# Kernel optimization log

Hardware: AMD Instinct MI355X
Metric: run time of the kernel (lower is better)

Reference implementation:

```python
import jax, jax.numpy as jnp
import numpy as np
import math

B, C1, H, W, D, NH = 32, 128, 32, 32, 256, 8
KS = 9
GLOBAL_RATIO = 0.0005
K_CH = 8


def setup_inputs() -> dict:
    key = jax.random.key(0)
    ks = jax.random.split(key, 6)
    s = 1.0 / math.sqrt(D)
    return {
        "x": jax.random.normal(ks[0], (B, 1, H, W), jnp.float32),
        "conv_w": jax.random.normal(ks[1], (C1, 1, KS, KS), jnp.float32) * 0.05,
        "channel_embed": jax.random.normal(ks[2], (C1, D), jnp.float32),
        "in_proj_w": jax.random.normal(ks[3], (3 * D, D), jnp.float32) * s,
        "in_proj_b": jnp.zeros((3 * D,), jnp.float32),
        "out_proj_w": jax.random.normal(ks[4], (D, D), jnp.float32) * s,
        "out_proj_b": jnp.zeros((D,), jnp.float32),
    }


def _pos_encoding(h, w, d):
    # Faithful to the torch code: the (H, d/2) sin/cos source broadcasts against
    # the trailing (W, d/2) dims of the (H,W,d/2) slice, so the PE varies only
    # along the W axis (requires H == W, which holds here).
    div = jnp.exp(jnp.arange(0, d, 2, dtype=jnp.float32) * (-math.log(10000.0) / d))
    ang = jnp.arange(w, dtype=jnp.float32)[:, None] * div          # (W, d/2)
    pe_w = jnp.stack([jnp.sin(ang), jnp.cos(ang)], axis=-1).reshape(w, d)
    return jnp.broadcast_to(pe_w[None], (h, w, d))                 # (H, W, d)


def _forward(x, conv_w, channel_embed, in_proj_w, in_proj_b, out_proj_w, out_proj_b):
    A = jax.nn.relu(jax.lax.conv_general_dilated(
        x, conv_w, window_strides=(1, 1),
        padding=[(KS // 2, KS // 2), (KS // 2, KS // 2)],
        dimension_numbers=("NCHW", "OIHW", "NCHW")))                # (B,C,H,W)
    Bb, C, Hh, Ww = A.shape
    k = max(1, int(math.ceil(GLOBAL_RATIO * C * Hh * Ww)))          # = 66

    # global top-k threshold mask over flattened activations
    A_flat = A.reshape(Bb, -1)
    topk_vals, _ = jax.lax.top_k(A_flat, k)
    thresh = topk_vals[:, -1][:, None]
    mask_global = (A_flat >= thresh).reshape(A.shape)
    A_global = A * mask_global.astype(A.dtype)

    # per-pixel channel top-8 + scatter
    v = jnp.transpose(A_global, (0, 2, 3, 1))                       # (B,H,W,C)
    topv, topi = jax.lax.top_k(v, K_CH)                             # (B,H,W,8)
    logits = (jax.nn.one_hot(topi, C, dtype=v.dtype) * topv[..., None]).sum(axis=-2)

    # global max normalization per batch element
    gmax = jnp.max(logits.reshape(Bb, -1), axis=1)[:, None, None, None]
    denom = jnp.where(gmax == 0, jnp.float32(1.0), gmax)
    sparse_weights = jnp.where(gmax == 0, jnp.float32(0.0), logits / denom)

    # channel-embedding projection + 2D positional encoding
    loc_emb = jnp.einsum('bhwc,cd->bhwd', sparse_weights, channel_embed)
    loc_emb = loc_emb + _pos_encoding(Hh, Ww, D)[None]
    seq = loc_emb.reshape(Bb, Hh * Ww, D)                           # (B, S, D)

    # nn.MultiheadAttention (batch_first) self-attention
    qkv = seq @ in_proj_w.T + in_proj_b
    q, kk, vv = jnp.split(qkv, 3, axis=-1)
    dh = D // NH
    heads = lambda t: t.reshape(Bb, -1, NH, dh).transpose(0, 2, 1, 3)
    q, kk, vv = heads(q), heads(kk), heads(vv)
    scores = jnp.einsum('bhqd,bhkd->bhqk', q, kk) / math.sqrt(dh)
    attn = jax.nn.softmax(scores, axis=-1)
    ctx = jnp.einsum('bhqk,bhkd->bhqd', attn, vv)
    ctx = ctx.transpose(0, 2, 1, 3).reshape(Bb, -1, D)
    attn_out = ctx @ out_proj_w.T + out_proj_b                      # (B, S, D)

    pooled = attn_out.mean(axis=1)                                  # (B, D)
    return pooled, sparse_weights, topi


def reference(x, conv_w, channel_embed, in_proj_w, in_proj_b, out_proj_w, out_proj_b):
    return _forward(x, conv_w, channel_embed, in_proj_w, in_proj_b,
                    out_proj_w, out_proj_b)
```

## Files before the change

### kernel.cpp

```cpp
#include <hip/hip_runtime.h>
#include <hip/hip_bf16.h>

#define BB 32
#define C1 128
#define SS 1024
#define DD 256
#define NHH 8
#define DHH 32
#define KSEL 66
#define TRIPLE 768
#define NTOK 80
#define SCAPS 128
#define CCAP 2048
#define DMAX (32 + NTOK)
#define PEROW (BB * NTOK)
#define SELFLAG 0x40000000u

typedef __attribute__((ext_vector_type(8))) short bf16x8;
typedef __attribute__((ext_vector_type(4))) float f32x4;

__device__ inline short f2bf(float f) {
  union { __hip_bfloat16 h; unsigned short u; } c;
  c.h = __float2bfloat16(f);
  return (short)c.u;
}
__device__ inline float pe_val(int w, int d) {
  int i2 = d >> 1;
  float dv = expf((float)(2 * i2) * (-9.210340371976184f / 256.f));
  float ang = (float)w * dv;
  return (d & 1) ? cosf(ang) : sinf(ang);
}

__global__ __launch_bounds__(256) void conv_relu_hist_kernel(
    const float* __restrict__ x, const float* __restrict__ w, float* __restrict__ A,
    unsigned* __restrict__ ghist_priv, unsigned* __restrict__ gmaxpriv,
    float* __restrict__ out_topi, float* __restrict__ out_sw,
    float* __restrict__ E) {
  const int bx = blockIdx.x;
  const int b = bx >> 6, c0 = (bx & 63) * 2;
  __shared__ float xs[40 * 40];
  __shared__ unsigned h[2048];
  __shared__ unsigned smax;
  const int t = threadIdx.x;
  {
    float4 z = {0.f, 0.f, 0.f, 0.f};
    float4* sw4 = (float4*)(out_sw + (size_t)bx * 2048);
    sw4[t] = z;
    sw4[t + 256] = z;
  }
  if (bx < 256) {
    int k0 = bx * 1024 + t * 4;
    float4 v = (k0 & 4) ? make_float4(4.f, 5.f, 6.f, 7.f)
                        : make_float4(0.f, 1.f, 2.f, 3.f);
    *(float4*)&out_topi[k0] = v;
  }
  if (bx < 32) E[(size_t)(PEROW + bx) * DD + t] = pe_val(bx, t);
  for (int i = t; i < 1600; i += 256) {
    int r = i / 40, cc = i - r * 40;
    int gi = r - 4, gj = cc - 4;
    float v = 0.f;
    if (gi >= 0 && gi < 32 && gj >= 0 && gj < 32) v = x[(size_t)b * 1024 + gi * 32 + gj];
    xs[i] = v;
  }
  for (int i = t; i < 2048; i += 256) h[i] = 0u;
  if (t == 0) smax = 0u;
  __syncthreads();
  const float* w0 = w + (size_t)c0 * 81;
  const float* w1 = w0 + 81;
  const int r = t >> 3, cbase = (t & 7) * 4;
  const float4* xs4 = (const float4*)xs;
  float a0 = 0.f, a1 = 0.f, a2 = 0.f, a3 = 0.f;
  float b0 = 0.f, b1 = 0.f, b2 = 0.f, b3 = 0.f;
#pragma unroll
  for (int u = 0; u < 9; ++u) {
    int base4 = (r + u) * 10 + (t & 7);
    float4 xA = xs4[base4];
    float4 xB = xs4[base4 + 1];
    float4 xC = xs4[base4 + 2];
    float xv[12] = {xA.x, xA.y, xA.z, xA.w, xB.x, xB.y, xB.z, xB.w,
                    xC.x, xC.y, xC.z, xC.w};
#pragma unroll
    for (int v = 0; v < 9; ++v) {
      float f0 = w0[u * 9 + v], f1 = w1[u * 9 + v];
      a0 += f0 * xv[v];     a1 += f0 * xv[v + 1];
      a2 += f0 * xv[v + 2]; a3 += f0 * xv[v + 3];
      b0 += f1 * xv[v];     b1 += f1 * xv[v + 1];
      b2 += f1 * xv[v + 2]; b3 += f1 * xv[v + 3];
    }
  }
  a0 = fmaxf(a0, 0.f); a1 = fmaxf(a1, 0.f); a2 = fmaxf(a2, 0.f); a3 = fmaxf(a3, 0.f);
  b0 = fmaxf(b0, 0.f); b1 = fmaxf(b1, 0.f); b2 = fmaxf(b2, 0.f); b3 = fmaxf(b3, 0.f);
  float4 va = {a0, a1, a2, a3}, vb = {b0, b1, b2, b3};
  *(float4*)&A[((size_t)(b * C1 + c0) << 10) + r * 32 + cbase] = va;
  *(float4*)&A[((size_t)(b * C1 + c0 + 1) << 10) + r * 32 + cbase] = vb;
  unsigned lmax = 0u;
#pragma unroll
  for (int k = 0; k < 8; ++k) {
    float f = (k == 0) ? a0 : (k == 1) ? a1 : (k == 2) ? a2 : (k == 3) ? a3
            : (k == 4) ? b0 : (k == 5) ? b1 : (k == 6) ? b2 : b3;
    unsigned bits = __float_as_uint(f);
    if (bits > lmax) lmax = bits;
    if (bits >= (1u << 21)) atomicAdd(&h[bits >> 21], 1u);
  }
  atomicMax(&smax, lmax);
  __syncthreads();
  {
    uint4* dst = (uint4*)(ghist_priv + (size_t)bx * 2048);
    const uint4* src = (const uint4*)h;
    dst[t] = src[t];
    dst[t + 256] = src[t + 256];
  }
  if (t == 0) gmaxpriv[bx] = smax;
}

__global__ __launch_bounds__(1024) void sel_kernel(
    const unsigned* __restrict__ ghist_priv, const unsigned* __restrict__ gmaxpriv,
    unsigned* __restrict__ selv, unsigned* __restrict__ gmaxb,
    unsigned* __restrict__ cnd_n, float* __restrict__ ctx) {
  const int b = blockIdx.x, t = threadIdx.x;
  __shared__ unsigned hl[2048];
  __shared__ unsigned sfx[1024];
  __shared__ unsigned gmx;
  if (t < 256) ctx[b * DD + t] = 0.f;
  if (t == 0) { cnd_n[b * 32] = 0u; gmx = 0u; }
  __syncthreads();
  if (t < 64) atomicMax(&gmx, gmaxpriv[b * 64 + t]);
  {
    const unsigned* base = ghist_priv + (size_t)b * 64 * 2048;
    unsigned s0 = 0, s1 = 0;
#pragma unroll 4
    for (int s = 0; s < 64; ++s) {
      s0 += base[s * 2048 + t];
      s1 += base[s * 2048 + t + 1024];
    }
    hl[t] = s0;
    hl[t + 1024] = s1;
  }
  __syncthreads();
  if (t == 0) gmaxb[b] = gmx;
  unsigned r = (unsigned)KSEL;
  sfx[t] = hl[2 * t] + hl[2 * t + 1];
  __syncthreads();
  for (int off = 1; off < 1024; off <<= 1) {
    unsigned v = (t + off < 1024) ? sfx[t + off] : 0u;
    __syncthreads();
    sfx[t] += v;
    __syncthreads();
  }
  if (sfx[0] < r) {
    if (t == 0) selv[b] = SELFLAG;
    return;
  }
  unsigned Snext = (t < 1023) ? sfx[t + 1] : 0u;
  unsigned hi = hl[2 * t + 1], lo = hl[2 * t];
  if (Snext < r && Snext + hi >= r) selv[b] = (unsigned)(2 * t + 1);
  else if (Snext + hi < r && Snext + hi + lo >= r) selv[b] = (unsigned)(2 * t);
}

__global__ __launch_bounds__(256) void gather_kernel(
    const float* __restrict__ A, const unsigned* __restrict__ selv,
    unsigned* __restrict__ cnd_n, float* __restrict__ candv,
    unsigned* __restrict__ candloc) {
  const int b = blockIdx.y, slice = blockIdx.x, t = threadIdx.x;
  const unsigned v1 = selv[b];
  if (v1 == SELFLAG) return;
  const unsigned thr = v1 << 21;
  __shared__ float lv[512];
  __shared__ unsigned ll[512];
  __shared__ unsigned lcnt, gbase;
  if (t == 0) lcnt = 0u;
  __syncthreads();
  const float4* Ab = (const float4*)(A + (size_t)b * (C1 * SS) + slice * 2048);
  const float4 va = Ab[t];
  const float4 vb = Ab[t + 256];
  const int base = slice * 2048 + t * 4;
  const float f[8] = {va.x, va.y, va.z, va.w, vb.x, vb.y, vb.z, vb.w};
#pragma unroll
  for (int c = 0; c < 8; ++c) {
    if (__float_as_uint(f[c]) >= thr) {
      unsigned loc = (unsigned)(base + (c < 4 ? c : 1020 + c));
      unsigned s = atomicAdd(&lcnt, 1u);
      if (s < 512u) {
        lv[s] = f[c];
        ll[s] = loc;
      } else {
        unsigned g = atomicAdd(&cnd_n[b * 32], 1u);
        if (g < (unsigned)CCAP) {
          candv[b * CCAP + g] = f[c];
          candloc[b * CCAP + g] = loc;
        }
      }
    }
  }
  __syncthreads();
  const unsigned cnt = lcnt < 512u ? lcnt : 512u;
  if (t == 0 && cnt) gbase = atomicAdd(&cnd_n[b * 32], cnt);
  __syncthreads();
  for (unsigned u = t; u < cnt; u += 256) {
    unsigned s = gbase + u;
    if (s < (unsigned)CCAP) {
      candv[b * CCAP + s] = lv[u];
      candloc[b * CCAP + s] = ll[u];
    }
  }
}

__global__ __launch_bounds__(256) void sparse_pixels_kernel(
    const unsigned* __restrict__ cnd_n, const float* __restrict__ candv,
    const unsigned* __restrict__ candloc, const unsigned* __restrict__ selv,
    const float* __restrict__ gmaxp, float* __restrict__ out_sw,
    float* __restrict__ out_topi, int* __restrict__ kidx8,
    float* __restrict__ kval8, unsigned* __restrict__ glist,
    unsigned* __restrict__ nswb, unsigned* __restrict__ npix) {
  const int b = blockIdx.x, t = threadIdx.x;
  __shared__ float cv[CCAP];
  __shared__ unsigned cl[CCAP];
  __shared__ float sv[SCAPS];
  __shared__ int sch[SCAPS], spx[SCAPS];
  __shared__ int s_n_sh;
  __shared__ unsigned pixbit[32];
  __shared__ int mcount[NTOK];
  __shared__ int leadp[NTOK];
  if (t == 0) s_n_sh = 0;
  if (t < 32) pixbit[t] = 0u;
  unsigned n = cnd_n[b * 32];
  if (n > (unsigned)CCAP) n = (unsigned)CCAP;
  const bool ok = (selv[b] != SELFLAG) && (n >= (unsigned)KSEL);
  for (unsigned i = t; i < n; i += 256) {
    cv[i] = candv[b * CCAP + i];
    cl[i] = candloc[b * CCAP + i];
  }
  __syncthreads();
  if (ok) {
    for (unsigned i = t; i < n; i += 256) {
      float v = cv[i];
      int g = 0;
      for (unsigned j = 0; j < n; ++j) g += (cv[j] > v);
      if (g < KSEL) {
        int k = atomicAdd(&s_n_sh, 1);
        if (k < SCAPS) {
          sv[k] = v;
          sch[k] = (int)(cl[i] >> 10);
          spx[k] = (int)(cl[i] & 1023u);
        }
      }
    }
  }
  __syncthreads();
  const int s_n = s_n_sh < SCAPS ? s_n_sh : SCAPS;
  for (int i = t; i < s_n; i += 256)
    atomicOr(&pixbit[spx[i] >> 5], 1u << (spx[i] & 31));
  __syncthreads();
  if (t == 0) {
    int np = 0;
#pragma unroll
    for (int wd = 0; wd < 32; ++wd) np += __popc(pixbit[wd]);
    npix[b] = (unsigned)(np < NTOK ? np : NTOK);
  }
  if (t < 32) {
    unsigned cnt = 0;
#pragma unroll
    for (int rr = 0; rr < 32; ++rr) cnt += (pixbit[rr] >> t) & 1u;
    nswb[b * 32 + t] = cnt;
  }
  const float gm = gmaxp[b];
  const float scale = gm > 0.f ? 1.f / gm : 0.f;
  __syncthreads();
  for (int i = t; i < s_n; i += 256) {
    const int p = spx[i];
    const float v = sv[i];
    const int c = sch[i];
    const int word = p >> 5, bit = p & 31;
    int slot = 0;
    for (int wd = 0; wd < word; ++wd) slot += __popc(pixbit[wd]);
    slot += __popc(pixbit[word] & (bit ? ((1u << bit) - 1u) : 0u));
    if (slot >= NTOK) continue;
    int rank = 0, cntp = 0;
    for (int j = 0; j < s_n; ++j) {
      if (spx[j] != p) continue;
      ++cntp;
      rank += (sv[j] > v || (sv[j] == v && sch[j] < c));
    }
    const size_t pix = (size_t)b * SS + p;
    const float sval = v * scale;
    if (rank < 8) {
      out_topi[pix * 8 + rank] = (float)c;
      out_sw[pix * C1 + c] = sval;
      kidx8[((size_t)b * NTOK + slot) * 8 + rank] = c;
      kval8[((size_t)b * NTOK + slot) * 8 + rank] = sval;
    }
    if (rank == 0) {
      glist[b * NTOK + slot] =
          ((unsigned)b << 16) | ((unsigned)slot << 8) | (unsigned)(p & 31);
      mcount[slot] = cntp < 8 ? cntp : 8;
      leadp[slot] = p;
    }
  }
  __syncthreads();
  const int np = (int)npix[b];
  for (int s = t; s < np; s += 256) {
    const int m = mcount[s];
    if (m >= 8) continue;
    const int p = leadp[s];
    int used[8];
    for (int k = 0; k < m; ++k) used[k] = kidx8[((size_t)b * NTOK + s) * 8 + k];
    int fill_c = 0;
    for (int j = m; j < 8; ++j) {
      bool adv = true;
      while (adv) {
        adv = false;
        for (int k = 0; k < m; ++k)
          if (used[k] == fill_c) adv = true;
        if (adv) ++fill_c;
      }
      kidx8[((size_t)b * NTOK + s) * 8 + j] = fill_c;
      kval8[((size_t)b * NTOK + s) * 8 + j] = 0.f;
      out_topi[((size_t)b * SS + p) * 8 + j] = (float)fill_c;
      ++fill_c;
    }
  }
}

__global__ __launch_bounds__(256) void emb_build_kernel(
    const unsigned* __restrict__ npix, const int* __restrict__ kidx8,
    const float* __restrict__ kval8, const unsigned* __restrict__ glist,
    const float* __restrict__ emb, float* __restrict__ E) {
  const int bx = blockIdx.x;
  const int d = threadIdx.x;
  const int b = bx / NTOK, i = bx - b * NTOK;
  if ((unsigned)i >= npix[b]) return;
  const int w = (int)(glist[bx] & 255u);
  const int* ki = kidx8 + (size_t)bx * 8;
  const float* kv = kval8 + (size_t)bx * 8;
  float e = pe_val(w, d);
#pragma unroll
  for (int j = 0; j < 8; ++j) e += kv[j] * emb[(size_t)ki[j] * DD + d];
  E[(size_t)bx * DD + d] = e;
}

__global__ __launch_bounds__(256) void eqkv_gemm_kernel(
    const float* __restrict__ E, const float* __restrict__ W,
    const float* __restrict__ bias, float* __restrict__ SQKV) {
  __shared__ __align__(16) short As[128][40];
  __shared__ __align__(16) short Bs[128][40];
  const int mt = blockIdx.x / 6, nt = blockIdx.x % 6;
  const int t = threadIdx.x;
  const int wv = t >> 6, lane = t & 63, lg = lane >> 4, ln = lane & 15;
  const int wm = wv >> 1, wn = wv & 1;

  f32x4 acc[4][4];
#pragma unroll
  for (int i = 0; i < 4; ++i)
#pragma unroll
    for (int j = 0; j < 4; ++j) acc[i][j] = (f32x4){0, 0, 0, 0};

  for (int k0 = 0; k0 < DD; k0 += 32) {
    __syncthreads();
    for (int f = t; f < 1024; f += 256) {
      int row = f >> 3, q4 = (f & 7) * 4;
      float4 xa = *(const float4*)&E[(size_t)(mt * 128 + row) * DD + k0 + q4];
      float4 wa = *(const float4*)&W[(size_t)(nt * 128 + row) * DD + k0 + q4];
      short* ad = &As[row][q4];
      ad[0] = f2bf(xa.x); ad[1] = f2bf(xa.y); ad[2] = f2bf(xa.z); ad[3] = f2bf(xa.w);
      short* bd = &Bs[row][q4];
      bd[0] = f2bf(wa.x); bd[1] = f2bf(wa.y); bd[2] = f2bf(wa.z); bd[3] = f2bf(wa.w);
    }
    __syncthreads();
    bf16x8 af[4], bfr[4];
#pragma unroll
    for (int i = 0; i < 4; ++i) af[i] = *(const bf16x8*)&As[wm * 64 + i * 16 + ln][lg * 8];
#pragma unroll
    for (int j = 0; j < 4; ++j) bfr[j] = *(const bf16x8*)&Bs[wn * 64 + j * 16 + ln][lg * 8];
#pragma unroll
    for (int i = 0; i < 4; ++i)
#pragma unroll
      for (int j = 0; j < 4; ++j)
        acc[i][j] = __builtin_amdgcn_mfma_f32_16x16x32_bf16(af[i], bfr[j], acc[i][j], 0, 0, 0);
  }
#pragma unroll
  for (int i = 0; i < 4; ++i) {
#pragma unroll
    for (int j = 0; j < 4; ++j) {
      int col = nt * 128 + wn * 64 + j * 16 + ln;
      float bcol = bias[col];
#pragma unroll
      for (int r = 0; r < 4; ++r) {
        int row = mt * 128 + wm * 64 + i * 16 + lg * 4 + r;
        SQKV[(size_t)row * TRIPLE + col] = acc[i][j][r] + bcol;
      }
    }
  }
}

__global__ __launch_bounds__(256) void attn_small_kernel(
    const float* __restrict__ SQKV, const unsigned* __restrict__ npix,
    const unsigned* __restrict__ nswb, float* __restrict__ ctx_sum) {
  const int blk = blockIdx.x;
  const int qg = blk & 3, h = (blk >> 2) & 7, b = blk >> 5;
  const int nsb = (int)npix[b];
  const int D = 32 + nsb;
  if (qg * 32 >= D) return;
  const int t = threadIdx.x;
  __shared__ float Kh[DMAX][36];
  __shared__ float Vh[DMAX][36];
  __shared__ float cw[DMAX];
  __shared__ float sctx[32];
  const int hoff = h * DHH;
  for (int idx = t; idx < D * 32; idx += 256) {
    int j = idx >> 5, d = idx & 31;
    int row = (j < 32) ? (PEROW + j) : (b * NTOK + j - 32);
    const float* src = &SQKV[(size_t)row * TRIPLE];
    Kh[j][d] = src[DD + hoff + d];
    Vh[j][d] = src[2 * DD + hoff + d];
  }
  if (t < D) cw[t] = (t < 32) ? (float)(32 - (int)nswb[b * 32 + t]) : 1.0f;
  if (t < 32) sctx[t] = 0.f;
  __syncthreads();

  const int q = qg * 32 + (t >> 3);
  const int g = t & 7;
  const bool act = (q < D);
  float m = -1e30f, l = 0.f;
  float acc[32];
#pragma unroll
  for (int d = 0; d < 32; ++d) acc[d] = 0.f;
  if (act) {
    const float qsc = 0.25506973f;
    int qrow = (q < 32) ? (PEROW + q) : (b * NTOK + q - 32);
    const float* qsrc = &SQKV[(size_t)qrow * TRIPLE];
    float qv[32];
#pragma unroll
    for (int d = 0; d < 32; ++d) qv[d] = qsrc[hoff + d] * qsc;
#pragma unroll 1
    for (int j = g; j < D; j += 8) {
      float s = 0.f;
      const float* kr = &Kh[j][0];
#pragma unroll
      for (int d = 0; d < 32; ++d) s += qv[d] * kr[d];
      float mn = fmaxf(m, s);
      float corr = exp2f(m - mn);
      float pw = cw[j] * exp2f(s - mn);
      l = l * corr + pw;
      const float* vr = &Vh[j][0];
#pragma unroll
      for (int d = 0; d < 32; ++d) acc[d] = acc[d] * corr + pw * vr[d];
      m = mn;
    }
  }
#pragma unroll
  for (int off = 1; off <= 4; off <<= 1) {
    float mo = __shfl_xor(m, off);
    float lo = __shfl_xor(l, off);
    float mm = fmaxf(m, mo);
    float fa = exp2f(m - mm), fb = exp2f(mo - mm);
    l = l * fa + lo * fb;
#pragma unroll
    for (int d = 0; d < 32; ++d) {
      float ao = __shfl_xor(acc[d], off);
      acc[d] = acc[d] * fa + ao * fb;
    }
    m = mm;
  }
  const float wq = (act && l > 0.f) ? cw[q] / l : 0.f;
#pragma unroll
  for (int d = 0; d < 32; ++d) {
    float val = wq * acc[d];
    val += __shfl_xor(val, 8);
    val += __shfl_xor(val, 16);
    val += __shfl_xor(val, 32);
    if ((t & 63) == 0) atomicAdd(&sctx[d], val);
  }
  __syncthreads();
  if (t < 32) atomicAdd(&ctx_sum[b * DD + hoff + t], sctx[t]);
}

__global__ __launch_bounds__(256) void pooled_kernel(
    const float* __restrict__ ctx_sum, const float* __restrict__ Wout,
    const float* __restrict__ bout, float* __restrict__ out) {
  const int b = blockIdx.x;
  const int o = threadIdx.x;
  __shared__ float mc[DD];
  mc[o] = ctx_sum[b * DD + o] * (1.f / 1024.f);
  __syncthreads();
  float acc = bout[o];
  const float* wr = Wout + (size_t)o * DD;
#pragma unroll 4
  for (int d = 0; d < DD; ++d) acc += mc[d] * wr[d];
  out[b * DD + o] = acc;
}

extern "C" void kernel_launch(void* const* d_in, const int* in_sizes, int n_in,
                              void* d_out, int out_size, void* d_ws, size_t ws_size,
                              hipStream_t stream) {
  const float* x = (const float*)d_in[0];
  const float* conv_w = (const float*)d_in[1];
  const float* emb = (const float*)d_in[2];
  const float* ipw = (const float*)d_in[3];
  const float* ipb = (const float*)d_in[4];
  const float* opw = (const float*)d_in[5];
  const float* opb = (const float*)d_in[6];

  float* out = (float*)d_out;
  float* out_pooled = out;
  float* out_sw = out + 8192;
  float* out_topi = out + 8192 + 4194304;

  char* ws = (char*)d_ws;
  float*    A       = (float*)(ws);
  unsigned* ghist_p = (unsigned*)(ws + 16777216);
  unsigned* gmaxpriv= (unsigned*)(ws + 33554432);
  unsigned* selv    = (unsigned*)(ws + 33562624);
  unsigned* gmaxb   = (unsigned*)(ws + 33562752);
  unsigned* nswb    = (unsigned*)(ws + 33562880);
  unsigned* npix    = (unsigned*)(ws + 33566976);
  unsigned* glist   = (unsigned*)(ws + 33567104);
  unsigned* cnd_n   = (unsigned*)(ws + 33577344);
  float*    candv   = (float*)(ws + 33581440);
  unsigned* candloc = (unsigned*)(ws + 33843584);
  int*      kidx8   = (int*)(ws + 34105728);
  float*    kval8   = (float*)(ws + 34187648);
  float*    E       = (float*)(ws + 34269568);
  float*    SQKV    = (float*)(ws + 37022080);
  float*    ctx     = (float*)(ws + 45279616);

  conv_relu_hist_kernel<<<BB * 64, 256, 0, stream>>>(x, conv_w, A, ghist_p, gmaxpriv,
                                                     out_topi, out_sw, E);
  sel_kernel<<<BB, 1024, 0, stream>>>(ghist_p, gmaxpriv, selv, gmaxb, cnd_n, ctx);
  gather_kernel<<<dim3(64, BB), 256, 0, stream>>>(A, selv, cnd_n, candv, candloc);
  sparse_pixels_kernel<<<BB, 256, 0, stream>>>(cnd_n, candv, candloc, selv,
                                               (const float*)gmaxb, out_sw, out_topi,
                                               kidx8, kval8, glist, nswb, npix);
  emb_build_kernel<<<PEROW, 256, 0, stream>>>(npix, kidx8, kval8, glist, emb, E);
  eqkv_gemm_kernel<<<21 * 6, 256, 0, stream>>>(E, ipw, ipb, SQKV);
  attn_small_kernel<<<BB * NHH * 4, 256, 0, stream>>>(SQKV, npix, nswb, ctx);
  pooled_kernel<<<BB, 256, 0, stream>>>(ctx, opw, opb, out_pooled);
}
```

Baseline: 120.4 us.

## Split histogram reduction into parallel kernel and skip gather slices below threshold

Moves the summing of the 64 per-slice private histograms out of sel_kernel, which ran only 32 blocks, into a new hist_reduce_kernel with 256 blocks, so the 16 MB of histogram reads spread across more CUs. sel_kernel now reads only the reduced 2048-bin histogram. gather_kernel also exits early for slices whose per-slice max lies below the selection threshold, which avoids reading A for most slices. The cost is one extra kernel launch and a small extra buffer, which shifts the workspace layout.

```diff
diff --git a/kernel.cpp b/kernel.cpp
--- a/kernel.cpp
+++ b/kernel.cpp
@@ -113,8 +113,19 @@
   if (t == 0) gmaxpriv[bx] = smax;
 }
 
+__global__ __launch_bounds__(256) void hist_reduce_kernel(
+    const unsigned* __restrict__ ghist_priv, unsigned* __restrict__ ghist_sum) {
+  const int p = blockIdx.x, b = blockIdx.y, t = threadIdx.x;
+  const int bin = p * 256 + t;
+  const unsigned* base = ghist_priv + (size_t)b * 64 * 2048 + bin;
+  unsigned s = 0;
+#pragma unroll 8
+  for (int sl = 0; sl < 64; ++sl) s += base[sl * 2048];
+  ghist_sum[b * 2048 + bin] = s;
+}
+
 __global__ __launch_bounds__(1024) void sel_kernel(
-    const unsigned* __restrict__ ghist_priv, const unsigned* __restrict__ gmaxpriv,
+    const unsigned* __restrict__ ghist_sum, const unsigned* __restrict__ gmaxpriv,
     unsigned* __restrict__ selv, unsigned* __restrict__ gmaxb,
     unsigned* __restrict__ cnd_n, float* __restrict__ ctx) {
   const int b = blockIdx.x, t = threadIdx.x;
@@ -125,17 +136,8 @@
   if (t == 0) { cnd_n[b * 32] = 0u; gmx = 0u; }
   __syncthreads();
   if (t < 64) atomicMax(&gmx, gmaxpriv[b * 64 + t]);
-  {
-    const unsigned* base = ghist_priv + (size_t)b * 64 * 2048;
-    unsigned s0 = 0, s1 = 0;
-#pragma unroll 4
-    for (int s = 0; s < 64; ++s) {
-      s0 += base[s * 2048 + t];
-      s1 += base[s * 2048 + t + 1024];
-    }
-    hl[t] = s0;
-    hl[t + 1024] = s1;
-  }
+  hl[t] = ghist_sum[b * 2048 + t];
+  hl[t + 1024] = ghist_sum[b * 2048 + t + 1024];
   __syncthreads();
   if (t == 0) gmaxb[b] = gmx;
   unsigned r = (unsigned)KSEL;
@@ -159,12 +161,14 @@
 
 __global__ __launch_bounds__(256) void gather_kernel(
     const float* __restrict__ A, const unsigned* __restrict__ selv,
+    const unsigned* __restrict__ gmaxpriv,
     unsigned* __restrict__ cnd_n, float* __restrict__ candv,
     unsigned* __restrict__ candloc) {
   const int b = blockIdx.y, slice = blockIdx.x, t = threadIdx.x;
   const unsigned v1 = selv[b];
   if (v1 == SELFLAG) return;
   const unsigned thr = v1 << 21;
+  if (gmaxpriv[b * 64 + slice] < thr) return;
   __shared__ float lv[512];
   __shared__ unsigned ll[512];
   __shared__ unsigned lcnt, gbase;
@@ -506,27 +510,29 @@
   float* out_topi = out + 8192 + 4194304;
 
   char* ws = (char*)d_ws;
-  float*    A       = (float*)(ws);
-  unsigned* ghist_p = (unsigned*)(ws + 16777216);
-  unsigned* gmaxpriv= (unsigned*)(ws + 33554432);
-  unsigned* selv    = (unsigned*)(ws + 33562624);
-  unsigned* gmaxb   = (unsigned*)(ws + 33562752);
-  unsigned* nswb    = (unsigned*)(ws + 33562880);
-  unsigned* npix    = (unsigned*)(ws + 33566976);
-  unsigned* glist   = (unsigned*)(ws + 33567104);
-  unsigned* cnd_n   = (unsigned*)(ws + 33577344);
-  float*    candv   = (float*)(ws + 33581440);
-  unsigned* candloc = (unsigned*)(ws + 33843584);
-  int*      kidx8   = (int*)(ws + 34105728);
-  float*    kval8   = (float*)(ws + 34187648);
-  float*    E       = (float*)(ws + 34269568);
-  float*    SQKV    = (float*)(ws + 37022080);
-  float*    ctx     = (float*)(ws + 45279616);
+  float*    A        = (float*)(ws);
+  unsigned* ghist_p  = (unsigned*)(ws + 16777216);
+  unsigned* ghist_s  = (unsigned*)(ws + 33554432);
+  unsigned* gmaxpriv = (unsigned*)(ws + 33816576);
+  unsigned* selv     = (unsigned*)(ws + 33824768);
+  unsigned* gmaxb    = (unsigned*)(ws + 33824896);
+  unsigned* nswb     = (unsigned*)(ws + 33825024);
+  unsigned* npix     = (unsigned*)(ws + 33829120);
+  unsigned* glist    = (unsigned*)(ws + 33829248);
+  unsigned* cnd_n    = (unsigned*)(ws + 33839488);
+  float*    candv    = (float*)(ws + 33843584);
+  unsigned* candloc  = (unsigned*)(ws + 34105728);
+  int*      kidx8    = (int*)(ws + 34367872);
+  float*    kval8    = (float*)(ws + 34449792);
+  float*    E        = (float*)(ws + 34531712);
+  float*    SQKV     = (float*)(ws + 37284224);
+  float*    ctx      = (float*)(ws + 45541760);
 
   conv_relu_hist_kernel<<<BB * 64, 256, 0, stream>>>(x, conv_w, A, ghist_p, gmaxpriv,
                                                      out_topi, out_sw, E);
-  sel_kernel<<<BB, 1024, 0, stream>>>(ghist_p, gmaxpriv, selv, gmaxb, cnd_n, ctx);
-  gather_kernel<<<dim3(64, BB), 256, 0, stream>>>(A, selv, cnd_n, candv, candloc);
+  hist_reduce_kernel<<<dim3(8, BB), 256, 0, stream>>>(ghist_p, ghist_s);
+  sel_kernel<<<BB, 1024, 0, stream>>>(ghist_s, gmaxpriv, selv, gmaxb, cnd_n, ctx);
+  gather_kernel<<<dim3(64, BB), 256, 0, stream>>>(A, selv, gmaxpriv, cnd_n, candv, candloc);
   sparse_pixels_kernel<<<BB, 256, 0, stream>>>(cnd_n, candv, candloc, selv,
                                                (const float*)gmaxb, out_sw, out_topi,
                                                kidx8, kval8, glist, nswb, npix);
```

New measurement: 122.5 us. No clear change (+1.8%).
